# Optimization experiments

Hardware: AMD Instinct MI355X
Metric: run time of the kernel (lower is better)

Reference implementation:

```python
import jax, jax.numpy as jnp
import numpy as np

B, H, W, C, HID, V, EMB = 16, 24, 96, 1024, 256, 5000, 256
BN_EPS = 1e-5


def _lin(k, fin, fout, s=0.05):
    return jax.random.normal(k, (fin, fout), jnp.float32) * s


def setup_inputs():
    ks = jax.random.split(jax.random.key(0), 24)
    inp = {
        "input_y": jax.random.randint(ks[0], (B,), 0, V),
        "input_hidden": jax.random.normal(ks[1], (B, 1, HID), jnp.float32),
        "img_feature": jax.random.normal(ks[2], (B, C, H, W), jnp.float32),
        "feature_w": W,
        "attention_sum": jnp.zeros((B, 1, H, W), jnp.float32),
        "alpha_t": jax.random.uniform(ks[3], (B, 1, H, W), jnp.float32),
        "feature_h": H,
        "batch_size": B,
        "h_mask": jax.random.randint(ks[4], (B,), 1, H + 1),
        "w_mask": jax.random.randint(ks[5], (B,), 1, W + 1),
        "emb_table": jax.random.normal(ks[6], (V, EMB), jnp.float32) * 0.05,
        "gru1_wi": _lin(ks[7], EMB, 3 * HID), "gru1_wh": _lin(ks[8], HID, 3 * HID),
        "gru1_bi": jnp.zeros((3 * HID,), jnp.float32), "gru1_bh": jnp.zeros((3 * HID,), jnp.float32),
        "fc1_w": _lin(ks[9], HID, 256), "fc1_b": jnp.zeros((256,), jnp.float32),
        "gru2_wi": _lin(ks[10], C, 3 * HID), "gru2_wh": _lin(ks[11], HID, 3 * HID),
        "gru2_bi": jnp.zeros((3 * HID,), jnp.float32), "gru2_bh": jnp.zeros((3 * HID,), jnp.float32),
        "out_w": _lin(ks[12], 128, V), "out_b": jnp.zeros((V,), jnp.float32),
        "emb2_w": _lin(ks[13], 256, 128), "emb2_b": jnp.zeros((128,), jnp.float32),
        "conv1_w": jax.random.normal(ks[14], (1, 1, 3, 3), jnp.float32) * 0.05,
        "conv1_b": jnp.zeros((1,), jnp.float32),
        "conv_tan_w": jax.random.normal(ks[15], (256, 256, 3, 3), jnp.float32) * 0.02,
        "conv_tan_b": jnp.zeros((256,), jnp.float32),
        "fc2_w": _lin(ks[16], HID, 128), "fc2_b": jnp.zeros((128,), jnp.float32),
        "ua_w": _lin(ks[17], C, 256), "ua_b": jnp.zeros((256,), jnp.float32),
        "uf_w": _lin(ks[18], 1, 256), "uf_b": jnp.zeros((256,), jnp.float32),
        "v_w": _lin(ks[19], 256, 1), "v_b": jnp.zeros((1,), jnp.float32),
        "wc_w": _lin(ks[20], C, 128), "wc_b": jnp.zeros((128,), jnp.float32),
        "bn1_gamma": jnp.ones((256,), jnp.float32), "bn1_beta": jnp.zeros((256,), jnp.float32),
        "bn1_mean": jnp.zeros((256,), jnp.float32), "bn1_var": jnp.ones((256,), jnp.float32),
    }
    return inp


def _gru(x, h, wi, wh, bi, bh):
    # PyTorch GRUCell semantics
    gi = x @ wi + bi
    gh = h @ wh + bh
    ir, iz, inn = jnp.split(gi, 3, axis=-1)
    hr, hz, hn = jnp.split(gh, 3, axis=-1)
    r = jax.nn.sigmoid(ir + hr)
    z = jax.nn.sigmoid(iz + hz)
    n = jnp.tanh(inn + r * hn)
    return (1.0 - z) * n + z * h


def _conv(x, w, b):
    y = jax.lax.conv_general_dilated(x, w, (1, 1), 'SAME',
                                     dimension_numbers=('NCHW', 'OIHW', 'NCHW'))
    return y + b[None, :, None, None]


def reference(input_y, input_hidden, img_feature, feature_w, attention_sum, alpha_t,
              feature_h, batch_size, h_mask, w_mask,
              emb_table, gru1_wi, gru1_wh, gru1_bi, gru1_bh, fc1_w, fc1_b,
              gru2_wi, gru2_wh, gru2_bi, gru2_bh, out_w, out_b, emb2_w, emb2_b,
              conv1_w, conv1_b, conv_tan_w, conv_tan_b, fc2_w, fc2_b,
              ua_w, ua_b, uf_w, uf_b, v_w, v_b, wc_w, wc_b,
              bn1_gamma, bn1_beta, bn1_mean, bn1_var):
    b, c, h, w = img_feature.shape
    # per-sample validity mask over the feature map  [B, H, W]
    et_mask = ((jnp.arange(h)[None, :] < h_mask[:, None])[:, :, None]
               & (jnp.arange(w)[None, :] < w_mask[:, None])[:, None, :]).astype(jnp.float32)

    emb = emb_table[input_y]                      # [B, 256] (dropout = identity, eval)
    h0 = input_hidden[:, 0, :]                    # [B, HID]
    st1 = _gru(emb, h0, gru1_wi, gru1_wh, gru1_bi, gru1_bh)
    st1 = st1 @ fc1_w + fc1_b                     # [B, 256]

    alpha_c = _conv(alpha_t, conv1_w, conv1_b)    # [B, 1, H, W]
    att_sum = attention_sum + alpha_c             # coverage accumulator

    img1 = jnp.einsum('bchw,cd->bhwd', img_feature, ua_w) + ua_b  # [B,H,W,256]
    att1 = att_sum[:, 0, :, :, None] * uf_w[0] + uf_b             # Linear(1,256)
    et = st1[:, None, None, :] + img1 + att1      # [B, H, W, 256]

    et_nchw = jnp.transpose(et, (0, 3, 1, 2))
    et_nchw = _conv(et_nchw, conv_tan_w, conv_tan_b)
    et_nchw = et_nchw * et_mask[:, None]
    inv = bn1_gamma / jnp.sqrt(bn1_var + BN_EPS)  # eval-mode BatchNorm2d(256)
    et_nchw = (et_nchw - bn1_mean[None, :, None, None]) * inv[None, :, None, None] \
              + bn1_beta[None, :, None, None]
    et_nchw = jnp.tanh(et_nchw)

    e = jnp.einsum('bchw,c->bhw', et_nchw, v_w[:, 0]) + v_b[0]    # [B, H, W]
    e_exp = jnp.exp(e) * et_mask
    e_sum = jnp.sum(e_exp, axis=(1, 2))
    alpha = e_exp / (e_sum[:, None, None] + 1e-8)                 # masked softmax

    ct = jnp.einsum('bhw,bchw->bc', alpha, img_feature)           # [B, 1024]
    st = _gru(ct, st1, gru2_wi, gru2_wh, gru2_bi, gru2_bh)        # [B, HID]
    hidden_next = st[:, None, :]

    pre = (st @ fc2_w + fc2_b) + (emb @ emb2_w + emb2_b) + (ct @ wc_w + wc_b)  # [B,128]
    output = jax.nn.log_softmax(pre @ out_w + out_b, axis=1)[:, None, :]       # [B,1,V]
    return output, hidden_next, alpha[:, None], att_sum
```

## Files before the change

kernel.cpp:

```cpp
#include <hip/hip_runtime.h>
#include <hip/hip_bf16.h>

#define B   16
#define H   24
#define W   96
#define C   1024
#define HID 256
#define V   5000
#define EMB 256
#define HW  (H*W)
#define BN_EPS 1e-5f
#define H2  (H+2)
#define W2  (W+2)

#define OUT0 0
#define OUT1 (B*V)
#define OUT2 (OUT1 + B*HID)
#define OUT3 (OUT2 + B*HW)

#define WSB_IMGT  0
#define WSB_ETP   75497472
#define WSB_WTB   96370688
#define WSB_UAT   97550336
#define WSB_E     98074624
#define WSB_ST1   98369536
#define WSB_CT    98385920
#define WSB_PRE   98451456
#define WSB_GIGH1 98459648
#define WSB_ST1G  98557952
#define WSB_GH2   98574336
#define WSB_GI2   98631680
#define WSB_STW   98861056

typedef __attribute__((ext_vector_type(8))) short short8;
typedef __attribute__((ext_vector_type(4))) float f32x4;

__device__ inline unsigned short f2bf(float f) {
    union { float f; unsigned int u; } v; v.f = f;
    unsigned int r = v.u + 0x7fffu + ((v.u >> 16) & 1u);
    return (unsigned short)(r >> 16);
}
__device__ inline float bf2f(unsigned short u) {
    union { unsigned int u; float f; } v; v.u = ((unsigned int)u) << 16;
    return v.f;
}

__global__ __launch_bounds__(256) void k_imgT(const float* img, unsigned short* imgT)
{
    int hw0 = blockIdx.x*128, c1 = blockIdx.y*128, b = blockIdx.z;
    int t = threadIdx.x;
    __shared__ unsigned short tr[128*136];
    #pragma unroll
    for (int i = 0; i < 16; ++i) {
        int flat = i*1024 + t*4;
        int r = flat >> 7;
        int col = flat & 127;
        float4 v = *(const float4*)&img[((size_t)(b*C + c1 + r))*HW + hw0 + col];
        tr[(col+0)*136 + r] = f2bf(v.x);
        tr[(col+1)*136 + r] = f2bf(v.y);
        tr[(col+2)*136 + r] = f2bf(v.z);
        tr[(col+3)*136 + r] = f2bf(v.w);
    }
    __syncthreads();
    #pragma unroll
    for (int i = 0; i < 8; ++i) {
        int flat = i*2048 + t*8;
        int orow = flat >> 7;
        int oc = flat & 127;
        *(short8*)&imgT[((size_t)(b*HW) + hw0 + orow)*1024 + c1 + oc] =
            *(const short8*)&tr[orow*136 + oc];
    }
}

__global__ __launch_bounds__(256) void k_attsum(
    const float* att_in, const float* alpha_t, const float* cw, const float* cb,
    float* att_out)
{
    int i = blockIdx.x*256 + threadIdx.x;
    int w = i % W; int h = (i / W) % H; int b = i / HW;
    float s = cb[0];
    #pragma unroll
    for (int kh = 0; kh < 3; ++kh) {
        int r = h + kh - 1; if (r < 0 || r >= H) continue;
        #pragma unroll
        for (int kw = 0; kw < 3; ++kw) {
            int c = w + kw - 1; if (c < 0 || c >= W) continue;
            s += alpha_t[(b*H + r)*W + c]*cw[kh*3+kw];
        }
    }
    att_out[i] = att_in[i] + s;
}

__global__ __launch_bounds__(256) void k_wtb(const float* src, unsigned short* dst)
{
    int idx = blockIdx.x*256 + threadIdx.x;
    int c = idx & 255; int o = (idx >> 8) & 255; int khw = idx >> 16;
    dst[(khw*256 + o)*256 + c] = f2bf(src[(o*256 + c)*9 + khw]);
}

__global__ __launch_bounds__(256) void k_uat(const float* src, unsigned short* dst)
{
    int idx = blockIdx.x*256 + threadIdx.x;
    int c = idx & 1023; int d = idx >> 10;
    dst[d*1024 + c] = f2bf(src[c*256 + d]);
}

__global__ __launch_bounds__(256) void k_zero(int4* p)
{
    p[blockIdx.x*256 + threadIdx.x] = make_int4(0,0,0,0);
}

__global__ __launch_bounds__(256) void k_tail1(
    const int* y, const float* emb_table, const float* h0,
    const float* wi, const float* wh, float* gigh)
{
    int virt = blockIdx.x*16;
    int t = threadIdx.x;
    bool gi_mode = virt < 768;
    __shared__ float a_l[16*256];
    for (int i = t; i < 4096; i += 256) {
        int b = i >> 8, k = i & 255;
        a_l[i] = gi_mode ? emb_table[y[b]*EMB + k] : h0[b*HID + k];
    }
    __syncthreads();
    int nl = t & 15, b = t >> 4;
    int n = (gi_mode ? virt : virt - 768) + nl;
    const float* wp = gi_mode ? wi : wh;
    float acc = 0.f;
    #pragma unroll 16
    for (int k = 0; k < 256; ++k) acc += a_l[b*256 + k]*wp[k*768 + n];
    gigh[b*1536 + virt + nl] = acc;
}

__global__ __launch_bounds__(256) void k_comb1(
    const float* gigh, const float* h0, const float* bi, const float* bh, float* st1g)
{
    int b = blockIdx.x, t = threadIdx.x;
    const float* g = gigh + b*1536;
    float ir = g[t] + bi[t], iz = g[256+t] + bi[256+t], in_ = g[512+t] + bi[512+t];
    float hr = g[768+t] + bh[t], hz = g[1024+t] + bh[256+t], hn = g[1280+t] + bh[512+t];
    float r = 1.f/(1.f+__expf(-(ir+hr)));
    float z = 1.f/(1.f+__expf(-(iz+hz)));
    float n = tanhf(in_ + r*hn);
    st1g[b*256+t] = (1.f - z)*n + z*h0[b*HID + t];
}

__global__ __launch_bounds__(256) void k_fc1s(
    const float* st1g, const float* fc1_w, const float* fc1_b, float* st1)
{
    int n0 = blockIdx.x*16, t = threadIdx.x;
    __shared__ float a_l[16*256];
    for (int i = t; i < 4096; i += 256) a_l[i] = st1g[i];
    __syncthreads();
    int nl = t & 15, b = t >> 4;
    float acc = fc1_b[n0+nl];
    #pragma unroll 16
    for (int k = 0; k < 256; ++k) acc += a_l[b*256+k]*fc1_w[k*256 + n0 + nl];
    st1[b*256 + n0 + nl] = acc;
}

__global__ __launch_bounds__(256, 3) void k_et(
    const unsigned short* imgT, const unsigned short* uat, const float* ua_b,
    const float* st1, const float* att_sum, const float* uf_w, const float* uf_b,
    unsigned short* et_p)
{
    int h = blockIdx.x, ny = blockIdx.y, b = blockIdx.z;
    int t = threadIdx.x;
    int wv = t >> 6, lane = t & 63, q = lane >> 4, ln = lane & 15;
    int n0 = ny*128 + wv*32;
    __shared__ __align__(16) unsigned short a_l[96*136];

    f32x4 acc[12];
    #pragma unroll
    for (int i = 0; i < 12; ++i) acc[i] = (f32x4){0.f,0.f,0.f,0.f};

    const unsigned short* ab = imgT + ((size_t)(b*HW) + h*W)*1024;
    const unsigned short* bbase = uat + (size_t)(n0 + ln)*1024 + q*8;

    for (int c0 = 0; c0 < 1024; c0 += 128) {
        __syncthreads();
        #pragma unroll
        for (int i = t; i < 1536; i += 256) {
            int m = i >> 4, j = i & 15;
            ((int4*)a_l)[m*17 + j] = *((const int4*)(ab + (size_t)m*1024 + c0) + j);
        }
        __syncthreads();
        #pragma unroll
        for (int cs = 0; cs < 128; cs += 32) {
            short8 av[6];
            #pragma unroll
            for (int mf = 0; mf < 6; ++mf)
                av[mf] = *(const short8*)&a_l[(ln + 16*mf)*136 + cs + q*8];
            #pragma unroll
            for (int j = 0; j < 2; ++j) {
                short8 bv = *(const short8*)(bbase + (size_t)(j*16)*1024 + c0 + cs);
                #pragma unroll
                for (int mf = 0; mf < 6; ++mf)
                    acc[mf*2+j] = __builtin_amdgcn_mfma_f32_16x16x32_bf16(av[mf], bv, acc[mf*2+j], 0, 0, 0);
            }
        }
    }

    float att_m[24];
    #pragma unroll
    for (int mf = 0; mf < 6; ++mf)
        #pragma unroll
        for (int r = 0; r < 4; ++r)
            att_m[mf*4+r] = att_sum[(b*H + h)*W + mf*16 + q*4 + r];
    #pragma unroll
    for (int j = 0; j < 2; ++j) {
        int n = n0 + j*16 + ln;
        float s1 = st1[b*256 + n] + ua_b[n];
        float ufw = uf_w[n], ufb = uf_b[n];
        #pragma unroll
        for (int mf = 0; mf < 6; ++mf)
            #pragma unroll
            for (int r = 0; r < 4; ++r) {
                int m = mf*16 + q*4 + r;
                float v = acc[mf*2+j][r] + s1 + att_m[mf*4+r]*ufw + ufb;
                et_p[((size_t)(b*H2 + h + 1)*W2 + (m + 1))*256 + n] = f2bf(v);
            }
    }
}

__global__ __launch_bounds__(256, 3) void k_conv(
    const unsigned short* et_p, const unsigned short* wtb, const float* cb,
    const float* bn_g, const float* bn_b, const float* bn_m, const float* bn_v,
    const float* v_w, float* e_part)
{
    int h = blockIdx.x, ny = blockIdx.y, b = blockIdx.z;
    int t = threadIdx.x;
    int wv = t >> 6, lane = t & 63, q = lane >> 4, ln = lane & 15;
    int n0 = ny*128 + wv*32;
    __shared__ __align__(16) unsigned short patch[3*98*72];
    __shared__ float lds_red[4][96];

    f32x4 acc[12];
    #pragma unroll
    for (int i = 0; i < 12; ++i) acc[i] = (f32x4){0.f,0.f,0.f,0.f};

    for (int c0 = 0; c0 < 256; c0 += 64) {
        __syncthreads();
        for (int i = t; i < 2352; i += 256) {
            int kh = i / 784; int r = i - kh*784; int x = r >> 3; int j = r & 7;
            const int4* src = (const int4*)et_p + ((size_t)(b*H2 + h + kh)*W2 + x)*32 + (c0 >> 3) + j;
            ((int4*)patch)[kh*882 + x*9 + j] = *src;
        }
        __syncthreads();
        #pragma unroll
        for (int kh = 0; kh < 3; ++kh) {
            #pragma unroll
            for (int kw = 0; kw < 3; ++kw) {
                const unsigned short* brow = wtb + ((size_t)((kh*3 + kw)*256 + n0 + ln))*256 + c0 + q*8;
                #pragma unroll
                for (int cs = 0; cs < 64; cs += 32) {
                    short8 av[6];
                    #pragma unroll
                    for (int mf = 0; mf < 6; ++mf)
                        av[mf] = *(const short8*)&patch[kh*7056 + (ln + 16*mf + kw)*72 + cs + q*8];
                    #pragma unroll
                    for (int j = 0; j < 2; ++j) {
                        short8 bv = *(const short8*)(brow + j*4096 + cs);
                        #pragma unroll
                        for (int mf = 0; mf < 6; ++mf)
                            acc[mf*2+j] = __builtin_amdgcn_mfma_f32_16x16x32_bf16(av[mf], bv, acc[mf*2+j], 0, 0, 0);
                    }
                }
            }
        }
    }

    float psum[24];
    #pragma unroll
    for (int i = 0; i < 24; ++i) psum[i] = 0.f;
    #pragma unroll
    for (int j = 0; j < 2; ++j) {
        int o = n0 + j*16 + ln;
        float inv  = bn_g[o]*rsqrtf(bn_v[o] + BN_EPS);
        float mean = bn_m[o], beta = bn_b[o], bias = cb[o], vw = v_w[o];
        #pragma unroll
        for (int mf = 0; mf < 6; ++mf)
            #pragma unroll
            for (int r = 0; r < 4; ++r) {
                float x = (acc[mf*2+j][r] + bias - mean)*inv + beta;
                x = fminf(fmaxf(x, -15.f), 15.f);
                float ex = __expf(2.f*x);
                psum[mf*4+r] += ((ex - 1.f)/(ex + 1.f))*vw;
            }
    }
    #pragma unroll
    for (int s = 1; s < 16; s <<= 1)
        #pragma unroll
        for (int i = 0; i < 24; ++i) psum[i] += __shfl_xor(psum[i], s);
    if (ln == 0) {
        #pragma unroll
        for (int mf = 0; mf < 6; ++mf)
            #pragma unroll
            for (int r = 0; r < 4; ++r)
                lds_red[wv][mf*16 + q*4 + r] = psum[mf*4+r];
    }
    __syncthreads();
    if (t < 96)
        e_part[(size_t)ny*(B*HW) + (b*H + h)*W + t] =
            lds_red[0][t] + lds_red[1][t] + lds_red[2][t] + lds_red[3][t];
}

__global__ __launch_bounds__(256) void k_softmax(
    const float* e_part, const int* h_mask, const int* w_mask, const float* v_b,
    float* alpha_out)
{
    int b = blockIdx.x, t = threadIdx.x;
    int hm = h_mask[b], wm = w_mask[b];
    float vb = v_b[0];
    __shared__ float red[256];
    float vals[9];
    float loc = 0.f;
    #pragma unroll
    for (int i = 0; i < 9; ++i) {
        int hw = t + i*256;
        int hh = hw / W, ww = hw % W;
        float v = 0.f;
        if (hh < hm && ww < wm)
            v = __expf(e_part[b*HW + hw] + e_part[B*HW + b*HW + hw] + vb);
        vals[i] = v; loc += v;
    }
    red[t] = loc; __syncthreads();
    for (int s = 128; s > 0; s >>= 1) { if (t < s) red[t] += red[t+s]; __syncthreads(); }
    float inv = 1.f/(red[0] + 1e-8f);
    #pragma unroll
    for (int i = 0; i < 9; ++i) alpha_out[b*HW + t + i*256] = vals[i]*inv;
}

__global__ __launch_bounds__(256) void k_ct0(float* ct)
{
    ct[blockIdx.x*256 + threadIdx.x] = 0.f;
}

__global__ __launch_bounds__(256) void k_ct(
    const float* alpha, const unsigned short* imgT, float* ct)
{
    int s = blockIdx.x, b = blockIdx.y, t = threadIdx.x;
    int cg = (t & 127)*8, half = t >> 7;
    float acc[8];
    #pragma unroll
    for (int j = 0; j < 8; ++j) acc[j] = 0.f;
    for (int i = 0; i < 96; ++i) {
        int hw = s*192 + i*2 + half;
        float a = alpha[b*HW + hw];
        union { short8 v; unsigned short u[8]; } pk;
        pk.v = *(const short8*)&imgT[((size_t)(b*HW) + hw)*1024 + cg];
        #pragma unroll
        for (int j = 0; j < 8; ++j) acc[j] += a*bf2f(pk.u[j]);
    }
    #pragma unroll
    for (int j = 0; j < 8; ++j) atomicAdd(&ct[b*1024 + cg + j], acc[j]);
}

__global__ __launch_bounds__(256) void k_gh2pe(
    const float* st1, const int* y, const float* emb_table,
    const float* wh, const float* emb2_w, float* gh2)
{
    int virt = blockIdx.x*16, t = threadIdx.x;
    bool ghm = virt < 768;
    __shared__ float a_l[16*256];
    for (int i = t; i < 4096; i += 256) {
        int b = i >> 8, k = i & 255;
        a_l[i] = ghm ? st1[b*256 + k] : emb_table[y[b]*EMB + k];
    }
    __syncthreads();
    int nl = t & 15, b = t >> 4;
    float acc = 0.f;
    if (ghm) {
        int n = virt + nl;
        #pragma unroll 16
        for (int k = 0; k < 256; ++k) acc += a_l[b*256+k]*wh[k*768 + n];
    } else {
        int n = virt - 768 + nl;
        #pragma unroll 16
        for (int k = 0; k < 256; ++k) acc += a_l[b*256+k]*emb2_w[k*128 + n];
    }
    gh2[b*896 + virt + nl] = acc;
}

__global__ __launch_bounds__(256) void k_gi2(
    const float* ct, const float* wi, const float* wc_w, float* gi2p)
{
    int virt = blockIdx.x*16, ks = blockIdx.y, t = threadIdx.x;
    int k0 = ks*256;
    __shared__ float a_l[16*256];
    for (int i = t; i < 4096; i += 256) {
        int b = i >> 8, k = i & 255;
        a_l[i] = ct[b*1024 + k0 + k];
    }
    __syncthreads();
    int nl = t & 15, b = t >> 4;
    float acc = 0.f;
    if (virt < 768) {
        int n = virt + nl;
        #pragma unroll 16
        for (int k = 0; k < 256; ++k) acc += a_l[b*256+k]*wi[(k0+k)*768 + n];
    } else {
        int n = virt - 768 + nl;
        #pragma unroll 16
        for (int k = 0; k < 256; ++k) acc += a_l[b*256+k]*wc_w[(k0+k)*128 + n];
    }
    gi2p[(ks*16 + b)*896 + virt + nl] = acc;
}

__global__ __launch_bounds__(256) void k_comb2(
    const float* gi2p, const float* gh2, const float* st1,
    const float* bi, const float* bh, float* hidden_out, float* st_ws)
{
    int b = blockIdx.x, t = threadIdx.x;
    float ir = bi[t], iz = bi[256+t], in_ = bi[512+t];
    #pragma unroll
    for (int ks = 0; ks < 4; ++ks) {
        const float* g = gi2p + (ks*16 + b)*896;
        ir += g[t]; iz += g[256+t]; in_ += g[512+t];
    }
    const float* gh = gh2 + b*896;
    float hr = gh[t] + bh[t], hz = gh[256+t] + bh[256+t], hn = gh[512+t] + bh[512+t];
    float h = st1[b*256+t];
    float r = 1.f/(1.f+__expf(-(ir+hr)));
    float z = 1.f/(1.f+__expf(-(iz+hz)));
    float n = tanhf(in_ + r*hn);
    float s = (1.f - z)*n + z*h;
    hidden_out[b*HID + t] = s;
    st_ws[b*256 + t] = s;
}

__global__ __launch_bounds__(256) void k_fc2s(
    const float* st_ws, const float* fc2_w, const float* fc2_b,
    const float* gh2, const float* emb2_b, const float* gi2p,
    const float* wc_b, float* pre)
{
    int n0 = blockIdx.x*16, t = threadIdx.x;
    __shared__ float a_l[16*256];
    for (int i = t; i < 4096; i += 256) a_l[i] = st_ws[i];
    __syncthreads();
    int nl = t & 15, b = t >> 4;
    int n = n0 + nl;
    float acc = fc2_b[n] + emb2_b[n] + wc_b[n] + gh2[b*896 + 768 + n];
    #pragma unroll
    for (int ks = 0; ks < 4; ++ks) acc += gi2p[(ks*16 + b)*896 + 768 + n];
    #pragma unroll 16
    for (int k = 0; k < 256; ++k) acc += a_l[b*256+k]*fc2_w[k*128 + n];
    pre[b*128 + n] = acc;
}

__global__ __launch_bounds__(256) void k_logits(
    const float* pre, const float* out_w, const float* out_b, float* out)
{
    int j0 = blockIdx.x*64, t = threadIdx.x;
    __shared__ float pre_l[16*128];
    for (int i = t; i < 2048; i += 256) pre_l[i] = pre[i];
    __syncthreads();
    int jl = t & 63, bg = t >> 6;
    int j = j0 + jl;
    if (j >= V) return;
    float acc0=0.f, acc1=0.f, acc2=0.f, acc3=0.f;
    const float* pl = pre_l + bg*4*128;
    #pragma unroll 8
    for (int k = 0; k < 128; ++k) {
        float wv = out_w[k*V + j];
        acc0 += pl[k]*wv; acc1 += pl[128+k]*wv; acc2 += pl[256+k]*wv; acc3 += pl[384+k]*wv;
    }
    float ob = out_b[j];
    out[(bg*4+0)*V + j] = acc0 + ob;
    out[(bg*4+1)*V + j] = acc1 + ob;
    out[(bg*4+2)*V + j] = acc2 + ob;
    out[(bg*4+3)*V + j] = acc3 + ob;
}

__global__ __launch_bounds__(1024) void k_lsm(float* out)
{
    int b = blockIdx.x, t = threadIdx.x;
    __shared__ float red[1024];
    float lg[5]; float mx = -1e30f;
    #pragma unroll
    for (int i = 0; i < 5; ++i) {
        int j = t + i*1024;
        lg[i] = (j < V) ? out[b*V + j] : -1e30f;
        mx = fmaxf(mx, lg[i]);
    }
    red[t] = mx; __syncthreads();
    for (int s = 512; s > 0; s >>= 1) { if (t < s) red[t] = fmaxf(red[t], red[t+s]); __syncthreads(); }
    float gmax = red[0]; __syncthreads();
    float se = 0.f;
    #pragma unroll
    for (int i = 0; i < 5; ++i) { int j = t + i*1024; if (j < V) se += __expf(lg[i] - gmax); }
    red[t] = se; __syncthreads();
    for (int s = 512; s > 0; s >>= 1) { if (t < s) red[t] += red[t+s]; __syncthreads(); }
    float lse = logf(red[0]);
    #pragma unroll
    for (int i = 0; i < 5; ++i) { int j = t + i*1024; if (j < V) out[b*V + j] = lg[i] - gmax - lse; }
}

extern "C" void kernel_launch(void* const* d_in, const int* in_sizes, int n_in,
                              void* d_out, int out_size, void* d_ws, size_t ws_size,
                              hipStream_t stream)
{
    const int*   input_y      = (const int*)  d_in[0];
    const float* input_hidden = (const float*)d_in[1];
    const float* img          = (const float*)d_in[2];
    const float* attention    = (const float*)d_in[4];
    const float* alpha_t      = (const float*)d_in[5];
    const int*   h_mask       = (const int*)  d_in[8];
    const int*   w_mask       = (const int*)  d_in[9];
    const float* emb_table    = (const float*)d_in[10];
    const float* gru1_wi      = (const float*)d_in[11];
    const float* gru1_wh      = (const float*)d_in[12];
    const float* gru1_bi      = (const float*)d_in[13];
    const float* gru1_bh      = (const float*)d_in[14];
    const float* fc1_w        = (const float*)d_in[15];
    const float* fc1_b        = (const float*)d_in[16];
    const float* gru2_wi      = (const float*)d_in[17];
    const float* gru2_wh      = (const float*)d_in[18];
    const float* gru2_bi      = (const float*)d_in[19];
    const float* gru2_bh      = (const float*)d_in[20];
    const float* out_w        = (const float*)d_in[21];
    const float* out_b        = (const float*)d_in[22];
    const float* emb2_w       = (const float*)d_in[23];
    const float* emb2_b       = (const float*)d_in[24];
    const float* conv1_w      = (const float*)d_in[25];
    const float* conv1_b      = (const float*)d_in[26];
    const float* conv_tan_w   = (const float*)d_in[27];
    const float* conv_tan_b   = (const float*)d_in[28];
    const float* fc2_w        = (const float*)d_in[29];
    const float* fc2_b        = (const float*)d_in[30];
    const float* ua_w         = (const float*)d_in[31];
    const float* ua_b         = (const float*)d_in[32];
    const float* uf_w         = (const float*)d_in[33];
    const float* uf_b         = (const float*)d_in[34];
    const float* v_w          = (const float*)d_in[35];
    const float* v_b          = (const float*)d_in[36];
    const float* wc_w         = (const float*)d_in[37];
    const float* wc_b         = (const float*)d_in[38];
    const float* bn1_gamma    = (const float*)d_in[39];
    const float* bn1_beta     = (const float*)d_in[40];
    const float* bn1_mean     = (const float*)d_in[41];
    const float* bn1_var      = (const float*)d_in[42];

    float* out = (float*)d_out;
    char*  ws  = (char*)d_ws;
    unsigned short* imgT = (unsigned short*)(ws + WSB_IMGT);
    unsigned short* et_p = (unsigned short*)(ws + WSB_ETP);
    unsigned short* wtb  = (unsigned short*)(ws + WSB_WTB);
    unsigned short* uat  = (unsigned short*)(ws + WSB_UAT);
    float* e_part = (float*)(ws + WSB_E);
    float* st1   = (float*)(ws + WSB_ST1);
    float* ct    = (float*)(ws + WSB_CT);
    float* pre   = (float*)(ws + WSB_PRE);
    float* gigh1 = (float*)(ws + WSB_GIGH1);
    float* st1g  = (float*)(ws + WSB_ST1G);
    float* gh2   = (float*)(ws + WSB_GH2);
    float* gi2p  = (float*)(ws + WSB_GI2);
    float* st_w  = (float*)(ws + WSB_STW);

    float* out_logits = out + OUT0;
    float* out_hidden = out + OUT1;
    float* out_alpha  = out + OUT2;
    float* out_attsum = out + OUT3;

    k_imgT<<<dim3(HW/128, C/128, B), 256, 0, stream>>>(img, imgT);
    k_tail1<<<96, 256, 0, stream>>>(input_y, emb_table, input_hidden,
                                    gru1_wi, gru1_wh, gigh1);
    k_comb1<<<B, 256, 0, stream>>>(gigh1, input_hidden, gru1_bi, gru1_bh, st1g);
    k_fc1s<<<16, 256, 0, stream>>>(st1g, fc1_w, fc1_b, st1);
    k_attsum<<<(B*HW)/256, 256, 0, stream>>>(attention, alpha_t, conv1_w, conv1_b, out_attsum);
    k_wtb<<<(9*256*256)/256, 256, 0, stream>>>(conv_tan_w, wtb);
    k_uat<<<(256*1024)/256, 256, 0, stream>>>(ua_w, uat);
    k_zero<<<(B*H2*W2*256/8)/256, 256, 0, stream>>>((int4*)et_p);
    k_et<<<dim3(H, 2, B), 256, 0, stream>>>(imgT, uat, ua_b, st1, out_attsum,
                                            uf_w, uf_b, et_p);
    k_conv<<<dim3(H, 2, B), 256, 0, stream>>>(et_p, wtb, conv_tan_b,
                                              bn1_gamma, bn1_beta, bn1_mean, bn1_var,
                                              v_w, e_part);
    k_softmax<<<B, 256, 0, stream>>>(e_part, h_mask, w_mask, v_b, out_alpha);
    k_ct0<<<(B*C)/256, 256, 0, stream>>>(ct);
    k_ct<<<dim3(12, B), 256, 0, stream>>>(out_alpha, imgT, ct);
    k_gh2pe<<<56, 256, 0, stream>>>(st1, input_y, emb_table, gru2_wh, emb2_w, gh2);
    k_gi2<<<dim3(56, 4), 256, 0, stream>>>(ct, gru2_wi, wc_w, gi2p);
    k_comb2<<<B, 256, 0, stream>>>(gi2p, gh2, st1, gru2_bi, gru2_bh, out_hidden, st_w);
    k_fc2s<<<8, 256, 0, stream>>>(st_w, fc2_w, fc2_b, gh2, emb2_b, gi2p, wc_b, pre);
    k_logits<<<(V + 63)/64, 256, 0, stream>>>(pre, out_w, out_b, out_logits);
    k_lsm<<<B, 1024, 0, stream>>>(out_logits);
}
```

Before: 565.0 us.

## Merge small prep and GRU-tail kernels to cut launches; zero only et_p borders

```diff
diff --git a/kernel.cpp b/kernel.cpp
--- a/kernel.cpp
+++ b/kernel.cpp
@@ -27,10 +27,8 @@
 #define WSB_CT    98385920
 #define WSB_PRE   98451456
 #define WSB_GIGH1 98459648
-#define WSB_ST1G  98557952
 #define WSB_GH2   98574336
 #define WSB_GI2   98631680
-#define WSB_STW   98861056
 
 typedef __attribute__((ext_vector_type(8))) short short8;
 typedef __attribute__((ext_vector_type(4))) float f32x4;
@@ -72,42 +70,52 @@
     }
 }
 
-__global__ __launch_bounds__(256) void k_attsum(
-    const float* att_in, const float* alpha_t, const float* cw, const float* cb,
-    float* att_out)
-{
-    int i = blockIdx.x*256 + threadIdx.x;
-    int w = i % W; int h = (i / W) % H; int b = i / HW;
-    float s = cb[0];
-    #pragma unroll
-    for (int kh = 0; kh < 3; ++kh) {
-        int r = h + kh - 1; if (r < 0 || r >= H) continue;
-        #pragma unroll
-        for (int kw = 0; kw < 3; ++kw) {
-            int c = w + kw - 1; if (c < 0 || c >= W) continue;
-            s += alpha_t[(b*H + r)*W + c]*cw[kh*3+kw];
-        }
-    }
-    att_out[i] = att_in[i] + s;
-}
-
-__global__ __launch_bounds__(256) void k_wtb(const float* src, unsigned short* dst)
-{
-    int idx = blockIdx.x*256 + threadIdx.x;
-    int c = idx & 255; int o = (idx >> 8) & 255; int khw = idx >> 16;
-    dst[(khw*256 + o)*256 + c] = f2bf(src[(o*256 + c)*9 + khw]);
-}
-
-__global__ __launch_bounds__(256) void k_uat(const float* src, unsigned short* dst)
-{
-    int idx = blockIdx.x*256 + threadIdx.x;
-    int c = idx & 1023; int d = idx >> 10;
-    dst[d*1024 + c] = f2bf(src[c*256 + d]);
-}
-
-__global__ __launch_bounds__(256) void k_zero(int4* p)
-{
-    p[blockIdx.x*256 + threadIdx.x] = make_int4(0,0,0,0);
+__global__ __launch_bounds__(256) void k_prep(
+    const float* conv_w_src, unsigned short* wtb,
+    const float* ua_w, unsigned short* uat,
+    const float* att_in, const float* alpha_t, const float* cw, const float* cb, float* att_out,
+    float* ct, unsigned short* et_p)
+{
+    int x = blockIdx.x, t = threadIdx.x;
+    if (x < 2304) {
+        int idx = x*256 + t;
+        int c = idx & 255; int o = (idx >> 8) & 255; int khw = idx >> 16;
+        wtb[(khw*256 + o)*256 + c] = f2bf(conv_w_src[(o*256 + c)*9 + khw]);
+    } else if (x < 3328) {
+        int idx = (x - 2304)*256 + t;
+        int c = idx & 1023; int d = idx >> 10;
+        uat[d*1024 + c] = f2bf(ua_w[c*256 + d]);
+    } else if (x < 3472) {
+        int i = (x - 3328)*256 + t;
+        int w = i % W; int h = (i / W) % H; int b = i / HW;
+        float s = cb[0];
+        #pragma unroll
+        for (int kh = 0; kh < 3; ++kh) {
+            int r = h + kh - 1; if (r < 0 || r >= H) continue;
+            #pragma unroll
+            for (int kw = 0; kw < 3; ++kw) {
+                int c = w + kw - 1; if (c < 0 || c >= W) continue;
+                s += alpha_t[(b*H + r)*W + c]*cw[kh*3+kw];
+            }
+        }
+        att_out[i] = att_in[i] + s;
+    } else if (x < 3536) {
+        ct[(x - 3472)*256 + t] = 0.f;
+    } else {
+        int flat = (x - 3536)*256 + t;
+        int b = flat / 7808; int r = flat - b*7808;
+        int h2, w2, j;
+        if (r < 3136)      { h2 = 0;  w2 = r >> 5;          j = r & 31; }
+        else if (r < 6272) { h2 = 25; w2 = (r - 3136) >> 5; j = (r - 3136) & 31; }
+        else {
+            int rr = r - 6272;
+            h2 = 1 + (rr >> 6);
+            int s = rr & 63;
+            w2 = (s < 32) ? 0 : 97;
+            j = s & 31;
+        }
+        ((int4*)et_p)[((size_t)(b*H2 + h2)*W2 + w2)*32 + j] = make_int4(0,0,0,0);
+    }
 }
 
 __global__ __launch_bounds__(256) void k_tail1(
@@ -132,25 +140,22 @@
     gigh[b*1536 + virt + nl] = acc;
 }
 
-__global__ __launch_bounds__(256) void k_comb1(
-    const float* gigh, const float* h0, const float* bi, const float* bh, float* st1g)
-{
-    int b = blockIdx.x, t = threadIdx.x;
-    const float* g = gigh + b*1536;
-    float ir = g[t] + bi[t], iz = g[256+t] + bi[256+t], in_ = g[512+t] + bi[512+t];
-    float hr = g[768+t] + bh[t], hz = g[1024+t] + bh[256+t], hn = g[1280+t] + bh[512+t];
-    float r = 1.f/(1.f+__expf(-(ir+hr)));
-    float z = 1.f/(1.f+__expf(-(iz+hz)));
-    float n = tanhf(in_ + r*hn);
-    st1g[b*256+t] = (1.f - z)*n + z*h0[b*HID + t];
-}
-
-__global__ __launch_bounds__(256) void k_fc1s(
-    const float* st1g, const float* fc1_w, const float* fc1_b, float* st1)
+__global__ __launch_bounds__(256) void k_fc1c(
+    const float* gigh, const float* h0, const float* bi, const float* bh,
+    const float* fc1_w, const float* fc1_b, float* st1)
 {
     int n0 = blockIdx.x*16, t = threadIdx.x;
     __shared__ float a_l[16*256];
-    for (int i = t; i < 4096; i += 256) a_l[i] = st1g[i];
+    for (int i = t; i < 4096; i += 256) {
+        int b = i >> 8, k = i & 255;
+        const float* g = gigh + b*1536;
+        float ir = g[k] + bi[k], iz = g[256+k] + bi[256+k], in_ = g[512+k] + bi[512+k];
+        float hr = g[768+k] + bh[k], hz = g[1024+k] + bh[256+k], hn = g[1280+k] + bh[512+k];
+        float r = 1.f/(1.f+__expf(-(ir+hr)));
+        float z = 1.f/(1.f+__expf(-(iz+hz)));
+        float n = tanhf(in_ + r*hn);
+        a_l[i] = (1.f - z)*n + z*h0[b*HID + k];
+    }
     __syncthreads();
     int nl = t & 15, b = t >> 4;
     float acc = fc1_b[n0+nl];
@@ -331,11 +336,6 @@
     for (int i = 0; i < 9; ++i) alpha_out[b*HW + t + i*256] = vals[i]*inv;
 }
 
-__global__ __launch_bounds__(256) void k_ct0(float* ct)
-{
-    ct[blockIdx.x*256 + threadIdx.x] = 0.f;
-}
-
 __global__ __launch_bounds__(256) void k_ct(
     const float* alpha, const unsigned short* imgT, float* ct)
 {
@@ -356,87 +356,83 @@
     for (int j = 0; j < 8; ++j) atomicAdd(&ct[b*1024 + cg + j], acc[j]);
 }
 
-__global__ __launch_bounds__(256) void k_gh2pe(
+__global__ __launch_bounds__(256) void k_g2(
     const float* st1, const int* y, const float* emb_table,
-    const float* wh, const float* emb2_w, float* gh2)
-{
-    int virt = blockIdx.x*16, t = threadIdx.x;
-    bool ghm = virt < 768;
+    const float* wh, const float* emb2_w, float* gh2,
+    const float* ct, const float* wi, const float* wc_w, float* gi2p)
+{
+    int x = blockIdx.x, t = threadIdx.x;
     __shared__ float a_l[16*256];
+    if (x < 56) {
+        int virt = x*16;
+        bool ghm = virt < 768;
+        for (int i = t; i < 4096; i += 256) {
+            int b = i >> 8, k = i & 255;
+            a_l[i] = ghm ? st1[b*256 + k] : emb_table[y[b]*EMB + k];
+        }
+        __syncthreads();
+        int nl = t & 15, b = t >> 4;
+        float acc = 0.f;
+        if (ghm) {
+            int n = virt + nl;
+            #pragma unroll 16
+            for (int k = 0; k < 256; ++k) acc += a_l[b*256+k]*wh[k*768 + n];
+        } else {
+            int n = virt - 768 + nl;
+            #pragma unroll 16
+            for (int k = 0; k < 256; ++k) acc += a_l[b*256+k]*emb2_w[k*128 + n];
+        }
+        gh2[b*896 + virt + nl] = acc;
+    } else {
+        int xx = x - 56;
+        int ks = xx / 56, virt = (xx - ks*56)*16;
+        int k0 = ks*256;
+        for (int i = t; i < 4096; i += 256) {
+            int b = i >> 8, k = i & 255;
+            a_l[i] = ct[b*1024 + k0 + k];
+        }
+        __syncthreads();
+        int nl = t & 15, b = t >> 4;
+        float acc = 0.f;
+        if (virt < 768) {
+            int n = virt + nl;
+            #pragma unroll 16
+            for (int k = 0; k < 256; ++k) acc += a_l[b*256+k]*wi[(k0+k)*768 + n];
+        } else {
+            int n = virt - 768 + nl;
+            #pragma unroll 16
+            for (int k = 0; k < 256; ++k) acc += a_l[b*256+k]*wc_w[(k0+k)*128 + n];
+        }
+        gi2p[(ks*16 + b)*896 + virt + nl] = acc;
+    }
+}
+
+__global__ __launch_bounds__(256) void k_fc2c(
+    const float* gi2p, const float* gh2, const float* st1,
+    const float* bi, const float* bh,
+    const float* fc2_w, const float* fc2_b, const float* emb2_b, const float* wc_b,
+    float* hidden_out, float* pre)
+{
+    int n0 = blockIdx.x*16, t = threadIdx.x;
+    __shared__ float st_l[16*256];
     for (int i = t; i < 4096; i += 256) {
         int b = i >> 8, k = i & 255;
-        a_l[i] = ghm ? st1[b*256 + k] : emb_table[y[b]*EMB + k];
-    }
-    __syncthreads();
-    int nl = t & 15, b = t >> 4;
-    float acc = 0.f;
-    if (ghm) {
-        int n = virt + nl;
-        #pragma unroll 16
-        for (int k = 0; k < 256; ++k) acc += a_l[b*256+k]*wh[k*768 + n];
-    } else {
-        int n = virt - 768 + nl;
-        #pragma unroll 16
-        for (int k = 0; k < 256; ++k) acc += a_l[b*256+k]*emb2_w[k*128 + n];
-    }
-    gh2[b*896 + virt + nl] = acc;
-}
-
-__global__ __launch_bounds__(256) void k_gi2(
-    const float* ct, const float* wi, const float* wc_w, float* gi2p)
-{
-    int virt = blockIdx.x*16, ks = blockIdx.y, t = threadIdx.x;
-    int k0 = ks*256;
-    __shared__ float a_l[16*256];
-    for (int i = t; i < 4096; i += 256) {
-        int b = i >> 8, k = i & 255;
-        a_l[i] = ct[b*1024 + k0 + k];
-    }
-    __syncthreads();
-    int nl = t & 15, b = t >> 4;
-    float acc = 0.f;
-    if (virt < 768) {
-        int n = virt + nl;
-        #pragma unroll 16
-        for (int k = 0; k < 256; ++k) acc += a_l[b*256+k]*wi[(k0+k)*768 + n];
-    } else {
-        int n = virt - 768 + nl;
-        #pragma unroll 16
-        for (int k = 0; k < 256; ++k) acc += a_l[b*256+k]*wc_w[(k0+k)*128 + n];
-    }
-    gi2p[(ks*16 + b)*896 + virt + nl] = acc;
-}
-
-__global__ __launch_bounds__(256) void k_comb2(
-    const float* gi2p, const float* gh2, const float* st1,
-    const float* bi, const float* bh, float* hidden_out, float* st_ws)
-{
-    int b = blockIdx.x, t = threadIdx.x;
-    float ir = bi[t], iz = bi[256+t], in_ = bi[512+t];
-    #pragma unroll
-    for (int ks = 0; ks < 4; ++ks) {
-        const float* g = gi2p + (ks*16 + b)*896;
-        ir += g[t]; iz += g[256+t]; in_ += g[512+t];
-    }
-    const float* gh = gh2 + b*896;
-    float hr = gh[t] + bh[t], hz = gh[256+t] + bh[256+t], hn = gh[512+t] + bh[512+t];
-    float h = st1[b*256+t];
-    float r = 1.f/(1.f+__expf(-(ir+hr)));
-    float z = 1.f/(1.f+__expf(-(iz+hz)));
-    float n = tanhf(in_ + r*hn);
-    float s = (1.f - z)*n + z*h;
-    hidden_out[b*HID + t] = s;
-    st_ws[b*256 + t] = s;
-}
-
-__global__ __launch_bounds__(256) void k_fc2s(
-    const float* st_ws, const float* fc2_w, const float* fc2_b,
-    const float* gh2, const float* emb2_b, const float* gi2p,
-    const float* wc_b, float* pre)
-{
-    int n0 = blockIdx.x*16, t = threadIdx.x;
-    __shared__ float a_l[16*256];
-    for (int i = t; i < 4096; i += 256) a_l[i] = st_ws[i];
+        float ir = bi[k], iz = bi[256+k], in_ = bi[512+k];
+        #pragma unroll
+        for (int ks = 0; ks < 4; ++ks) {
+            const float* g = gi2p + (ks*16 + b)*896;
+            ir += g[k]; iz += g[256+k]; in_ += g[512+k];
+        }
+        const float* gh = gh2 + b*896;
+        float hr = gh[k] + bh[k], hz = gh[256+k] + bh[256+k], hn = gh[512+k] + bh[512+k];
+        float h = st1[b*256+k];
+        float r = 1.f/(1.f+__expf(-(ir+hr)));
+        float z = 1.f/(1.f+__expf(-(iz+hz)));
+        float n = tanhf(in_ + r*hn);
+        float s = (1.f - z)*n + z*h;
+        st_l[i] = s;
+        if (blockIdx.x == 0) hidden_out[b*HID + k] = s;
+    }
     __syncthreads();
     int nl = t & 15, b = t >> 4;
     int n = n0 + nl;
@@ -444,7 +440,7 @@
     #pragma unroll
     for (int ks = 0; ks < 4; ++ks) acc += gi2p[(ks*16 + b)*896 + 768 + n];
     #pragma unroll 16
-    for (int k = 0; k < 256; ++k) acc += a_l[b*256+k]*fc2_w[k*128 + n];
+    for (int k = 0; k < 256; ++k) acc += st_l[b*256+k]*fc2_w[k*128 + n];
     pre[b*128 + n] = acc;
 }
 
@@ -552,10 +548,8 @@
     float* ct    = (float*)(ws + WSB_CT);
     float* pre   = (float*)(ws + WSB_PRE);
     float* gigh1 = (float*)(ws + WSB_GIGH1);
-    float* st1g  = (float*)(ws + WSB_ST1G);
     float* gh2   = (float*)(ws + WSB_GH2);
     float* gi2p  = (float*)(ws + WSB_GI2);
-    float* st_w  = (float*)(ws + WSB_STW);
 
     float* out_logits = out + OUT0;
     float* out_hidden = out + OUT1;
@@ -563,26 +557,24 @@
     float* out_attsum = out + OUT3;
 
     k_imgT<<<dim3(HW/128, C/128, B), 256, 0, stream>>>(img, imgT);
+    k_prep<<<4024, 256, 0, stream>>>(conv_tan_w, wtb, ua_w, uat,
+                                     attention, alpha_t, conv1_w, conv1_b, out_attsum,
+                                     ct, et_p);
     k_tail1<<<96, 256, 0, stream>>>(input_y, emb_table, input_hidden,
                                     gru1_wi, gru1_wh, gigh1);
-    k_comb1<<<B, 256, 0, stream>>>(gigh1, input_hidden, gru1_bi, gru1_bh, st1g);
-    k_fc1s<<<16, 256, 0, stream>>>(st1g, fc1_w, fc1_b, st1);
-    k_attsum<<<(B*HW)/256, 256, 0, stream>>>(attention, alpha_t, conv1_w, conv1_b, out_attsum);
-    k_wtb<<<(9*256*256)/256, 256, 0, stream>>>(conv_tan_w, wtb);
-    k_uat<<<(256*1024)/256, 256, 0, stream>>>(ua_w, uat);
-    k_zero<<<(B*H2*W2*256/8)/256, 256, 0, stream>>>((int4*)et_p);
+    k_fc1c<<<16, 256, 0, stream>>>(gigh1, input_hidden, gru1_bi, gru1_bh,
+                                   fc1_w, fc1_b, st1);
     k_et<<<dim3(H, 2, B), 256, 0, stream>>>(imgT, uat, ua_b, st1, out_attsum,
                                             uf_w, uf_b, et_p);
     k_conv<<<dim3(H, 2, B), 256, 0, stream>>>(et_p, wtb, conv_tan_b,
                                               bn1_gamma, bn1_beta, bn1_mean, bn1_var,
                                               v_w, e_part);
     k_softmax<<<B, 256, 0, stream>>>(e_part, h_mask, w_mask, v_b, out_alpha);
-    k_ct0<<<(B*C)/256, 256, 0, stream>>>(ct);
     k_ct<<<dim3(12, B), 256, 0, stream>>>(out_alpha, imgT, ct);
-    k_gh2pe<<<56, 256, 0, stream>>>(st1, input_y, emb_table, gru2_wh, emb2_w, gh2);
-    k_gi2<<<dim3(56, 4), 256, 0, stream>>>(ct, gru2_wi, wc_w, gi2p);
-    k_comb2<<<B, 256, 0, stream>>>(gi2p, gh2, st1, gru2_bi, gru2_bh, out_hidden, st_w);
-    k_fc2s<<<8, 256, 0, stream>>>(st_w, fc2_w, fc2_b, gh2, emb2_b, gi2p, wc_b, pre);
+    k_g2<<<280, 256, 0, stream>>>(st1, input_y, emb_table, gru2_wh, emb2_w, gh2,
+                                  ct, gru2_wi, wc_w, gi2p);
+    k_fc2c<<<8, 256, 0, stream>>>(gi2p, gh2, st1, gru2_bi, gru2_bh,
+                                  fc2_w, fc2_b, emb2_b, wc_b, out_hidden, pre);
     k_logits<<<(V + 63)/64, 256, 0, stream>>>(pre, out_w, out_b, out_logits);
     k_lsm<<<B, 1024, 0, stream>>>(out_logits);
 }
```

Measured after the change: 549.5 us. 1.03x faster.
